# Kernel tuning notes

Measured on AMD Instinct MI355X. Metric: run time of the kernel, lower is better.

Reference implementation:

```python
import jax, jax.numpy as jnp
import numpy as np

DIM = 2048
N_HEADS = 16
N_KV_HEADS = 4
HEAD_DIM = 128
SLIDING_WINDOW = 1024
ROPE_BASE = 10000.0


def _rotate_half(x):
    d = x.shape[-1] // 2
    return jnp.concatenate((-x[..., d:], x[..., :d]), axis=-1)


def _rope_cos_sin(T, dtype):
    inv_freq = 1.0 / (ROPE_BASE ** (jnp.arange(0, HEAD_DIM, 2, dtype=jnp.float32) / HEAD_DIM))
    t = jnp.arange(T, dtype=jnp.float32)
    freqs = jnp.outer(t, inv_freq)            # [T, HEAD_DIM//2]
    emb = jnp.concatenate((freqs, freqs), axis=-1)  # [T, HEAD_DIM]
    return jnp.cos(emb).astype(dtype), jnp.sin(emb).astype(dtype)


def setup_inputs() -> dict:
    key = jax.random.key(0)
    kx, kq, kk, kv, ko = jax.random.split(key, 5)
    s_in = 1.0 / np.sqrt(DIM)
    s_o = 1.0 / np.sqrt(N_HEADS * HEAD_DIM)
    return {
        "x": jax.random.normal(kx, (1, 4096, DIM), dtype=jnp.float32),
        "Wq": jax.random.normal(kq, (DIM, N_HEADS * HEAD_DIM), dtype=jnp.float32) * s_in,
        "Wk": jax.random.normal(kk, (DIM, N_KV_HEADS * HEAD_DIM), dtype=jnp.float32) * s_in,
        "Wv": jax.random.normal(kv, (DIM, N_KV_HEADS * HEAD_DIM), dtype=jnp.float32) * s_in,
        "Wo": jax.random.normal(ko, (N_HEADS * HEAD_DIM, DIM), dtype=jnp.float32) * s_o,
    }


def reference(x, Wq, Wk, Wv, Wo):
    B, T, C = x.shape
    # projections -> [B, H, T, D]
    q = (x @ Wq).reshape(B, T, N_HEADS, HEAD_DIM).transpose(0, 2, 1, 3)
    k = (x @ Wk).reshape(B, T, N_KV_HEADS, HEAD_DIM).transpose(0, 2, 1, 3)
    v = (x @ Wv).reshape(B, T, N_KV_HEADS, HEAD_DIM).transpose(0, 2, 1, 3)

    cos, sin = _rope_cos_sin(T, x.dtype)      # [T, D], broadcast over B, H
    q = q * cos + _rotate_half(q) * sin
    k = k * cos + _rotate_half(k) * sin

    # GQA: repeat kv heads (repeat_interleave over head axis)
    kv_rep = N_HEADS // N_KV_HEADS
    k = jnp.repeat(k, kv_rep, axis=1)
    v = jnp.repeat(v, kv_rep, axis=1)

    scale = 1.0 / np.sqrt(HEAD_DIM)
    att = jnp.einsum("bhqd,bhkd->bhqk", q, k) * scale  # [B, H, T, T]

    i = jnp.arange(T)[:, None]
    j = jnp.arange(T)[None, :]
    allowed = (j <= i) & ((i - j) < SLIDING_WINDOW)     # causal + sliding window
    att = jnp.where(allowed, att, -jnp.inf)
    att = jax.nn.softmax(att, axis=-1)

    y = jnp.einsum("bhqk,bhkd->bhqd", att, v)           # [B, H, T, D]
    y = y.transpose(0, 2, 1, 3).reshape(B, T, N_HEADS * HEAD_DIM)
    return y @ Wo
```

## Files before the change

kernel.cpp:

```cpp
#include <hip/hip_runtime.h>
#include <math.h>

typedef __bf16 bf16;
typedef __bf16 bf16x8 __attribute__((ext_vector_type(8)));
typedef __bf16 bf16x4 __attribute__((ext_vector_type(4)));
typedef float f32x4 __attribute__((ext_vector_type(4)));

__device__ __forceinline__ void ldg_lds16(const bf16* g, bf16* l) {
#if __has_builtin(__builtin_amdgcn_global_load_lds)
    __builtin_amdgcn_global_load_lds(
        (const __attribute__((address_space(1))) void*)g,
        (__attribute__((address_space(3))) void*)l, 16, 0, 0);
#else
    *(bf16x8*)l = *(const bf16x8*)g;
#endif
}

__global__ void cvt_x(const float* __restrict__ X, bf16* __restrict__ Xb, int total8)
{
    int idx = blockIdx.x * 256 + threadIdx.x;
    if (idx >= total8) return;
    const float* p = X + (size_t)idx * 8;
    f32x4 a = *reinterpret_cast<const f32x4*>(p);
    f32x4 b = *reinterpret_cast<const f32x4*>(p + 4);
    bf16x8 r;
    r[0] = (bf16)a[0]; r[1] = (bf16)a[1]; r[2] = (bf16)a[2]; r[3] = (bf16)a[3];
    r[4] = (bf16)b[0]; r[5] = (bf16)b[1]; r[6] = (bf16)b[2]; r[7] = (bf16)b[3];
    *reinterpret_cast<bf16x8*>(Xb + (size_t)idx * 8) = r;
}

__global__ void cvt_wt3(const float* __restrict__ Wq, const float* __restrict__ Wk,
                        const float* __restrict__ Wv, bf16* __restrict__ Wt)
{
    __shared__ float t[32][33];
    int bx = blockIdx.x;
    const float* W; int Ncols, nbase;
    if (bx < 64)      { W = Wq; Ncols = 2048; nbase = 0;    }
    else if (bx < 80) { W = Wk; Ncols = 512;  nbase = 2048; bx -= 64; }
    else              { W = Wv; Ncols = 512;  nbase = 2560; bx -= 80; }
    const int n0 = bx * 32, k0 = blockIdx.y * 32;
    const int x = threadIdx.x, y = threadIdx.y;
    #pragma unroll
    for (int i = 0; i < 4; ++i)
        t[y + 8 * i][x] = W[(size_t)(k0 + y + 8 * i) * Ncols + n0 + x];
    __syncthreads();
    #pragma unroll
    for (int i = 0; i < 4; ++i)
        Wt[(size_t)(nbase + n0 + y + 8 * i) * 2048 + k0 + x] = (bf16)t[x][y + 8 * i];
}

__global__ void cvt_wt(const float* __restrict__ W, bf16* __restrict__ Wt, int Ncols)
{
    __shared__ float t[32][33];
    const int n0 = blockIdx.x * 32, k0 = blockIdx.y * 32;
    const int x = threadIdx.x, y = threadIdx.y;
    #pragma unroll
    for (int i = 0; i < 4; ++i)
        t[y + 8 * i][x] = W[(size_t)(k0 + y + 8 * i) * Ncols + n0 + x];
    __syncthreads();
    #pragma unroll
    for (int i = 0; i < 4; ++i)
        Wt[(size_t)(n0 + y + 8 * i) * 2048 + k0 + x] = (bf16)t[x][y + 8 * i];
}

template <int MODE>
__global__ __launch_bounds__(256) void gemm_bt(
    const bf16* __restrict__ A, const bf16* __restrict__ Bt,
    void* __restrict__ C0, void* __restrict__ C1, void* __restrict__ C2,
    int M, int N, int K)
{
    __shared__ __align__(16) bf16 As[128 * 32];
    __shared__ __align__(16) bf16 Bs[128 * 32];

    const int tid  = threadIdx.x;
    const int lane = tid & 63;
    const int wave = tid >> 6;
    const int quad = lane >> 4;
    const int l16  = lane & 15;

    const int m0 = blockIdx.y * 128;
    const int n0 = blockIdx.x * 128;
    const int wm = (wave >> 1) * 64;
    const int wn = (wave & 1) * 64;

    f32x4 acc[4][4] = {};

    for (int k0 = 0; k0 < K; k0 += 32) {
        #pragma unroll
        for (int p = 0; p < 2; ++p) {
            int u = p * 256 + tid;
            int row = u >> 2, kc = u & 3;
            ldg_lds16(A  + (size_t)(m0 + row) * K + k0 + kc * 8, &As[u * 8]);
            ldg_lds16(Bt + (size_t)(n0 + row) * K + k0 + kc * 8, &Bs[u * 8]);
        }
        __syncthreads();

        bf16x8 af[4], bfr[4];
        #pragma unroll
        for (int i = 0; i < 4; ++i) {
            af[i]  = *reinterpret_cast<const bf16x8*>(&As[(wm + i * 16 + l16) * 32 + quad * 8]);
            bfr[i] = *reinterpret_cast<const bf16x8*>(&Bs[(wn + i * 16 + l16) * 32 + quad * 8]);
        }
        #pragma unroll
        for (int mi = 0; mi < 4; ++mi)
            #pragma unroll
            for (int ni = 0; ni < 4; ++ni)
                acc[mi][ni] = __builtin_amdgcn_mfma_f32_16x16x32_bf16(
                    af[mi], bfr[ni], acc[mi][ni], 0, 0, 0);
        __syncthreads();
    }

    #pragma unroll
    for (int mi = 0; mi < 4; ++mi) {
        #pragma unroll
        for (int ni = 0; ni < 4; ++ni) {
            const int row = m0 + wm + mi * 16 + quad * 4;
            const int col = n0 + wn + ni * 16 + l16;
            if (MODE == 2) {
                float* C = (float*)C0;
                #pragma unroll
                for (int r = 0; r < 4; ++r)
                    C[(size_t)(row + r) * N + col] = acc[mi][ni][r];
            } else {
                if (n0 < 2048) {
                    bf16* Q = (bf16*)C0;
                    #pragma unroll
                    for (int r = 0; r < 4; ++r)
                        Q[(size_t)(row + r) * 2048 + col] = (bf16)acc[mi][ni][r];
                } else if (n0 < 2560) {
                    bf16* Kb = (bf16*)C1;
                    #pragma unroll
                    for (int r = 0; r < 4; ++r)
                        Kb[(size_t)(row + r) * 512 + (col - 2048)] = (bf16)acc[mi][ni][r];
                } else {
                    bf16* Vt = (bf16*)C2;
                    bf16x4 v;
                    #pragma unroll
                    for (int r = 0; r < 4; ++r) v[r] = (bf16)acc[mi][ni][r];
                    *reinterpret_cast<bf16x4*>(&Vt[(size_t)(col - 2560) * 4096 + row]) = v;
                }
            }
        }
    }
}

__global__ __launch_bounds__(512, 2) void gemm256_qkv(
    const bf16* __restrict__ A, const bf16* __restrict__ Bt,
    bf16* __restrict__ Qo, bf16* __restrict__ Ko, bf16* __restrict__ Vt,
    int K)
{
    __shared__ __align__(16) bf16 smem[2 * 32768];

    const int tid  = threadIdx.x;
    const int lane = tid & 63;
    const int wave = tid >> 6;
    const int quad = lane >> 4;
    const int l16  = lane & 15;
    const int wm   = wave >> 2;
    const int wn   = wave & 3;

    const int m0 = blockIdx.y * 256;
    const int n0 = blockIdx.x * 256;

    int offA[4], offB[4];
    #pragma unroll
    for (int p = 0; p < 4; ++p) {
        int u = p * 512 + tid;
        int row = u >> 3;
        int kc8 = (u & 7) ^ (row & 7);
        offA[p] = (m0 + row) * K + kc8 * 8;
        offB[p] = (n0 + row) * K + kc8 * 8;
    }
    const int dstoff = tid * 8;

    const int xv = (l16 & 7) << 4;
    const int c0 = ((quad * 16) ^ xv) >> 1;
    const int c1 = ((64 + quad * 16) ^ xv) >> 1;
    const int rA = (wm * 128 + l16) * 64;
    const int rB = (wn * 64 + l16) * 64;

    f32x4 acc[8][4] = {};
    const int NT = K >> 6;

    {
        bf16* d0 = smem;
        bf16* d1 = smem + 32768;
        #pragma unroll
        for (int p = 0; p < 4; ++p) {
            ldg_lds16(A  + offA[p], d0 + p * 4096 + dstoff);
            ldg_lds16(Bt + offB[p], d0 + 16384 + p * 4096 + dstoff);
        }
        #pragma unroll
        for (int p = 0; p < 4; ++p) {
            ldg_lds16(A  + offA[p] + 64, d1 + p * 4096 + dstoff);
            ldg_lds16(Bt + offB[p] + 64, d1 + 16384 + p * 4096 + dstoff);
        }
    }
    asm volatile("s_waitcnt vmcnt(8)" ::: "memory");
    __builtin_amdgcn_sched_barrier(0);
    __builtin_amdgcn_s_barrier();
    __builtin_amdgcn_sched_barrier(0);

    for (int t = 0; t < NT; ++t) {
        const bf16* As = smem + (t & 1) * 32768;
        const bf16* Bs = As + 16384;

        bf16x8 a0[8], b0[4];
        #pragma unroll
        for (int i = 0; i < 8; ++i)
            a0[i] = *(const bf16x8*)(As + rA + i * 1024 + c0);
        #pragma unroll
        for (int i = 0; i < 4; ++i)
            b0[i] = *(const bf16x8*)(Bs + rB + i * 1024 + c0);

        #pragma unroll
        for (int mi = 0; mi < 8; ++mi)
            #pragma unroll
            for (int ni = 0; ni < 4; ++ni)
                acc[mi][ni] = __builtin_amdgcn_mfma_f32_16x16x32_bf16(
                    a0[mi], b0[ni], acc[mi][ni], 0, 0, 0);

        bf16x8 a1[8], b1[4];
        #pragma unroll
        for (int i = 0; i < 8; ++i)
            a1[i] = *(const bf16x8*)(As + rA + i * 1024 + c1);
        #pragma unroll
        for (int i = 0; i < 4; ++i)
            b1[i] = *(const bf16x8*)(Bs + rB + i * 1024 + c1);

        asm volatile("s_waitcnt lgkmcnt(0)" ::: "memory");
        __builtin_amdgcn_sched_barrier(0);
        __builtin_amdgcn_s_barrier();
        __builtin_amdgcn_sched_barrier(0);

        if (t + 2 < NT) {
            bf16* d = smem + (t & 1) * 32768;
            const int koff = (t + 2) * 64;
            #pragma unroll
            for (int p = 0; p < 4; ++p) {
                ldg_lds16(A  + offA[p] + koff, d + p * 4096 + dstoff);
                ldg_lds16(Bt + offB[p] + koff, d + 16384 + p * 4096 + dstoff);
            }
        }

        __builtin_amdgcn_s_setprio(1);
        #pragma unroll
        for (int mi = 0; mi < 8; ++mi)
            #pragma unroll
            for (int ni = 0; ni < 4; ++ni)
                acc[mi][ni] = __builtin_amdgcn_mfma_f32_16x16x32_bf16(
                    a1[mi], b1[ni], acc[mi][ni], 0, 0, 0);
        __builtin_amdgcn_s_setprio(0);

        if (t + 2 < NT) {
            asm volatile("s_waitcnt vmcnt(8)" ::: "memory");
            __builtin_amdgcn_sched_barrier(0);
            __builtin_amdgcn_s_barrier();
            __builtin_amdgcn_sched_barrier(0);
        } else if (t == NT - 2) {
            asm volatile("s_waitcnt vmcnt(0)" ::: "memory");
            __builtin_amdgcn_sched_barrier(0);
            __builtin_amdgcn_s_barrier();
            __builtin_amdgcn_sched_barrier(0);
        }
    }

    #pragma unroll
    for (int mi = 0; mi < 8; ++mi) {
        #pragma unroll
        for (int ni = 0; ni < 4; ++ni) {
            const int row = m0 + wm * 128 + mi * 16 + quad * 4;
            const int col = n0 + wn * 64 + ni * 16 + l16;
            if (n0 < 2048) {
                #pragma unroll
                for (int r = 0; r < 4; ++r)
                    Qo[(size_t)(row + r) * 2048 + col] = (bf16)acc[mi][ni][r];
            } else if (n0 < 2560) {
                #pragma unroll
                for (int r = 0; r < 4; ++r)
                    Ko[(size_t)(row + r) * 512 + (col - 2048)] = (bf16)acc[mi][ni][r];
            } else {
                bf16x4 v;
                #pragma unroll
                for (int r = 0; r < 4; ++r) v[r] = (bf16)acc[mi][ni][r];
                *reinterpret_cast<bf16x4*>(&Vt[(size_t)(col - 2560) * 4096 + row]) = v;
            }
        }
    }
}

__global__ void rope2_kernel(bf16* __restrict__ Qb, bf16* __restrict__ Kb,
                             int qtot, int ktot)
{
    int idx = blockIdx.x * 256 + threadIdx.x;
    bf16* base; int logH;
    if (idx < qtot) { base = Qb; logH = 4; }
    else {
        idx -= qtot;
        if (idx >= ktot) return;
        base = Kb; logH = 2;
    }
    int j  = idx & 63;
    int th = idx >> 6;
    int t  = th >> logH;

    bf16* p = base + (size_t)th * 128;
    const float NEG_LN1E4_64 = -0.14391155806323211f;
    float inv_freq = expf(NEG_LN1E4_64 * (float)j);
    float ang = (float)t * inv_freq;
    float c = cosf(ang), s = sinf(ang);
    float q0 = (float)p[j], q1 = (float)p[j + 64];
    p[j]      = (bf16)(q0 * c - q1 * s);
    p[j + 64] = (bf16)(q1 * c + q0 * s);
}

__global__ __launch_bounds__(256) void attn_v7(
    const bf16* __restrict__ Q, const bf16* __restrict__ K,
    const bf16* __restrict__ Vt, bf16* __restrict__ Y)
{
    const float scale = 0.08838834764831845f;

    __shared__ __align__(16) bf16 Ks[2 * 64 * 128];
    __shared__ __align__(16) bf16 Vs[2 * 128 * 64];
    __shared__ __align__(16) bf16 Pl[4][16 * 72];

    const int tid  = threadIdx.x;
    const int lane = tid & 63;
    const int wave = tid >> 6;
    const int quad = lane >> 4;
    const int l16  = lane & 15;

    const int i0  = blockIdx.x * 64;
    const int h   = blockIdx.y;
    const int kvh = h >> 2;
    const int q0  = i0 + wave * 16;
    bf16* Plw = Pl[wave];

    bf16x8 qf[4];
    {
        const bf16* qp = Q + (size_t)(q0 + l16) * 2048 + h * 128 + quad * 8;
        #pragma unroll
        for (int c = 0; c < 4; ++c)
            qf[c] = *reinterpret_cast<const bf16x8*>(qp + c * 32);
    }

    f32x4 o[8] = {};
    float lsum[4] = {0.f, 0.f, 0.f, 0.f};

    const int ks = (i0 >= 1024) ? (i0 - 1024) : 0;
    const int nsteps = (i0 + 64 - ks) >> 6;

    auto stage = [&](int tt, int bsel) {
        const int k0s = ks + tt * 64;
        bf16* kd = Ks + bsel * 8192;
        bf16* vd = Vs + bsel * 8192;
        #pragma unroll
        for (int p = 0; p < 4; ++p) {
            int u = p * 256 + tid;
            int kk = u >> 4, sc = u & 15;
            ldg_lds16(K + (size_t)(k0s + kk) * 512 + kvh * 128 + (sc ^ (kk & 15)) * 8,
                      kd + u * 8);
        }
        #pragma unroll
        for (int p = 0; p < 4; ++p) {
            int u = p * 256 + tid;
            int d = u >> 3, sc = u & 7;
            ldg_lds16(Vt + (size_t)(kvh * 128 + d) * 4096 + k0s + (sc ^ (d & 7)) * 8,
                      vd + u * 8);
        }
    };

    stage(0, 0);
    stage(1, 1);
    asm volatile("s_waitcnt vmcnt(8)" ::: "memory");
    __builtin_amdgcn_sched_barrier(0);
    __builtin_amdgcn_s_barrier();
    __builtin_amdgcn_sched_barrier(0);

    for (int t = 0; t < nsteps; ++t) {
        const int b  = t & 1;
        const int k0 = ks + t * 64;
        const bf16* Kb = Ks + b * 8192;
        const bf16* Vb = Vs + b * 8192;

        f32x4 s[4];
        __builtin_amdgcn_s_setprio(1);
        #pragma unroll
        for (int kh = 0; kh < 4; ++kh) {
            const int kk = kh * 16 + l16;
            f32x4 sv = {};
            #pragma unroll
            for (int c = 0; c < 4; ++c) {
                bf16x8 kf = *reinterpret_cast<const bf16x8*>(
                    &Kb[kk * 128 + (((c * 4 + quad) ^ (kk & 15)) * 8)]);
                sv = __builtin_amdgcn_mfma_f32_16x16x32_bf16(qf[c], kf, sv, 0, 0, 0);
            }
            s[kh] = sv;
        }
        __builtin_amdgcn_s_setprio(0);

        #pragma unroll
        for (int kh = 0; kh < 4; ++kh) {
            const int key = k0 + kh * 16 + l16;
            #pragma unroll
            for (int r = 0; r < 4; ++r) {
                const int qrow = q0 + quad * 4 + r;
                bool ok = (unsigned)(qrow - key) < 1024u;
                float pv = ok ? __expf(s[kh][r] * scale) : 0.f;
                lsum[r] += pv;
                Plw[(quad * 4 + r) * 72 + kh * 16 + l16] = (bf16)pv;
            }
        }

        bf16x8 pf0 = *reinterpret_cast<const bf16x8*>(&Plw[l16 * 72 + quad * 8]);
        bf16x8 pf1 = *reinterpret_cast<const bf16x8*>(&Plw[l16 * 72 + 32 + quad * 8]);
        __builtin_amdgcn_s_setprio(1);
        #pragma unroll
        for (int n = 0; n < 8; ++n) {
            const int d = n * 16 + l16;
            bf16x8 v0 = *reinterpret_cast<const bf16x8*>(
                &Vb[d * 64 + (((quad) ^ (d & 7)) * 8)]);
            bf16x8 v1 = *reinterpret_cast<const bf16x8*>(
                &Vb[d * 64 + (((4 + quad) ^ (d & 7)) * 8)]);
            o[n] = __builtin_amdgcn_mfma_f32_16x16x32_bf16(pf0, v0, o[n], 0, 0, 0);
            o[n] = __builtin_amdgcn_mfma_f32_16x16x32_bf16(pf1, v1, o[n], 0, 0, 0);
        }
        __builtin_amdgcn_s_setprio(0);

        asm volatile("s_waitcnt lgkmcnt(0)" ::: "memory");
        __builtin_amdgcn_sched_barrier(0);
        __builtin_amdgcn_s_barrier();
        __builtin_amdgcn_sched_barrier(0);

        if (t + 2 < nsteps) {
            stage(t + 2, b);
            asm volatile("s_waitcnt vmcnt(8)" ::: "memory");
        } else {
            asm volatile("s_waitcnt vmcnt(0)" ::: "memory");
        }
        __builtin_amdgcn_sched_barrier(0);
        __builtin_amdgcn_s_barrier();
        __builtin_amdgcn_sched_barrier(0);
    }

    #pragma unroll
    for (int r = 0; r < 4; ++r) {
        #pragma unroll
        for (int off = 1; off < 16; off <<= 1)
            lsum[r] += __shfl_xor(lsum[r], off, 64);
    }
    #pragma unroll
    for (int r = 0; r < 4; ++r) {
        int row = q0 + quad * 4 + r;
        float inv = (lsum[r] > 0.f) ? 1.f / lsum[r] : 0.f;
        #pragma unroll
        for (int n = 0; n < 8; ++n)
            Y[(size_t)row * 2048 + h * 128 + n * 16 + l16] = (bf16)(o[n][r] * inv);
    }
}

extern "C" void kernel_launch(void* const* d_in, const int* in_sizes, int n_in,
                              void* d_out, int out_size, void* d_ws, size_t ws_size,
                              hipStream_t stream)
{
    const float* x  = (const float*)d_in[0];
    const float* Wq = (const float*)d_in[1];
    const float* Wk = (const float*)d_in[2];
    const float* Wv = (const float*)d_in[3];
    const float* Wo = (const float*)d_in[4];
    float* out = (float*)d_out;

    const int T = 4096, DIM = 2048;

    char* po = (char*)d_out;
    bf16* Qb = (bf16*)(po);
    bf16* Kb = (bf16*)(po + (16u << 20));
    bf16* Vtb = (bf16*)(po + (20u << 20));

    char* ws = (char*)d_ws;
    bf16* xb    = (bf16*)(ws);
    bf16* Wqkvt = (bf16*)(ws + (16u << 20));
    bf16* Yb    = (bf16*)(ws);
    bf16* Wot   = (bf16*)(ws + (16u << 20));

    cvt_x<<<dim3(T * DIM / 8 / 256), 256, 0, stream>>>(x, xb, T * DIM / 8);

    dim3 tb(32, 8);
    cvt_wt3<<<dim3(96, 64), tb, 0, stream>>>(Wq, Wk, Wv, Wqkvt);

    gemm256_qkv<<<dim3(3072 / 256, T / 256), 512, 0, stream>>>(
        xb, Wqkvt, Qb, Kb, Vtb, DIM);

    cvt_wt<<<dim3(2048 / 32, 64), tb, 0, stream>>>(Wo, Wot, 2048);

    int qtot = T * 16 * 64, ktot = T * 4 * 64;
    rope2_kernel<<<(qtot + ktot + 255) / 256, 256, 0, stream>>>(Qb, Kb, qtot, ktot);

    attn_v7<<<dim3(T / 64, 16), 256, 0, stream>>>(Qb, Kb, Vtb, Yb);

    gemm_bt<2><<<dim3(2048 / 128, T / 128), 256, 0, stream>>>(
        Yb, Wot, out, nullptr, nullptr, T, 2048, DIM);
}
```

Baseline: 317.3 us.

## Replace output projection GEMM with double-buffered swizzled 256x128 kernel; reverse attention block order

The output projection moves from a simple single-buffered 128x128 GEMM to a 512-thread 256x128 tile kernel. The new kernel uses a 64-wide K step, an XOR-swizzled LDS layout, double buffering with direct global-to-LDS loads, and explicit waitcnt/barrier scheduling with setprio around the MFMA blocks. The aim is to hide global load latency and cut LDS bank conflicts. The attention kernel also launches query tiles in reverse order, so the longer sliding-window blocks are scheduled first and tail imbalance shrinks. The larger tile halves the grid to 256 blocks and raises register and LDS pressure.

```diff
diff --git a/kernel.cpp b/kernel.cpp
--- a/kernel.cpp
+++ b/kernel.cpp
@@ -61,87 +61,6 @@
     #pragma unroll
     for (int i = 0; i < 4; ++i)
         Wt[(size_t)(n0 + y + 8 * i) * 2048 + k0 + x] = (bf16)t[x][y + 8 * i];
-}
-
-template <int MODE>
-__global__ __launch_bounds__(256) void gemm_bt(
-    const bf16* __restrict__ A, const bf16* __restrict__ Bt,
-    void* __restrict__ C0, void* __restrict__ C1, void* __restrict__ C2,
-    int M, int N, int K)
-{
-    __shared__ __align__(16) bf16 As[128 * 32];
-    __shared__ __align__(16) bf16 Bs[128 * 32];
-
-    const int tid  = threadIdx.x;
-    const int lane = tid & 63;
-    const int wave = tid >> 6;
-    const int quad = lane >> 4;
-    const int l16  = lane & 15;
-
-    const int m0 = blockIdx.y * 128;
-    const int n0 = blockIdx.x * 128;
-    const int wm = (wave >> 1) * 64;
-    const int wn = (wave & 1) * 64;
-
-    f32x4 acc[4][4] = {};
-
-    for (int k0 = 0; k0 < K; k0 += 32) {
-        #pragma unroll
-        for (int p = 0; p < 2; ++p) {
-            int u = p * 256 + tid;
-            int row = u >> 2, kc = u & 3;
-            ldg_lds16(A  + (size_t)(m0 + row) * K + k0 + kc * 8, &As[u * 8]);
-            ldg_lds16(Bt + (size_t)(n0 + row) * K + k0 + kc * 8, &Bs[u * 8]);
-        }
-        __syncthreads();
-
-        bf16x8 af[4], bfr[4];
-        #pragma unroll
-        for (int i = 0; i < 4; ++i) {
-            af[i]  = *reinterpret_cast<const bf16x8*>(&As[(wm + i * 16 + l16) * 32 + quad * 8]);
-            bfr[i] = *reinterpret_cast<const bf16x8*>(&Bs[(wn + i * 16 + l16) * 32 + quad * 8]);
-        }
-        #pragma unroll
-        for (int mi = 0; mi < 4; ++mi)
-            #pragma unroll
-            for (int ni = 0; ni < 4; ++ni)
-                acc[mi][ni] = __builtin_amdgcn_mfma_f32_16x16x32_bf16(
-                    af[mi], bfr[ni], acc[mi][ni], 0, 0, 0);
-        __syncthreads();
-    }
-
-    #pragma unroll
-    for (int mi = 0; mi < 4; ++mi) {
-        #pragma unroll
-        for (int ni = 0; ni < 4; ++ni) {
-            const int row = m0 + wm + mi * 16 + quad * 4;
-            const int col = n0 + wn + ni * 16 + l16;
-            if (MODE == 2) {
-                float* C = (float*)C0;
-                #pragma unroll
-                for (int r = 0; r < 4; ++r)
-                    C[(size_t)(row + r) * N + col] = acc[mi][ni][r];
-            } else {
-                if (n0 < 2048) {
-                    bf16* Q = (bf16*)C0;
-                    #pragma unroll
-                    for (int r = 0; r < 4; ++r)
-                        Q[(size_t)(row + r) * 2048 + col] = (bf16)acc[mi][ni][r];
-                } else if (n0 < 2560) {
-                    bf16* Kb = (bf16*)C1;
-                    #pragma unroll
-                    for (int r = 0; r < 4; ++r)
-                        Kb[(size_t)(row + r) * 512 + (col - 2048)] = (bf16)acc[mi][ni][r];
-                } else {
-                    bf16* Vt = (bf16*)C2;
-                    bf16x4 v;
-                    #pragma unroll
-                    for (int r = 0; r < 4; ++r) v[r] = (bf16)acc[mi][ni][r];
-                    *reinterpret_cast<bf16x4*>(&Vt[(size_t)(col - 2560) * 4096 + row]) = v;
-                }
-            }
-        }
-    }
 }
 
 __global__ __launch_bounds__(512, 2) void gemm256_qkv(
@@ -289,6 +208,137 @@
     }
 }
 
+__global__ __launch_bounds__(512, 2) void gemm_out(
+    const bf16* __restrict__ A, const bf16* __restrict__ Bt,
+    float* __restrict__ C, int K)
+{
+    __shared__ __align__(16) bf16 smem[2 * 24576];
+
+    const int tid  = threadIdx.x;
+    const int lane = tid & 63;
+    const int wave = tid >> 6;
+    const int quad = lane >> 4;
+    const int l16  = lane & 15;
+    const int wm   = wave >> 1;
+    const int wn   = wave & 1;
+
+    const int m0 = blockIdx.y * 256;
+    const int n0 = blockIdx.x * 128;
+
+    int offA[4], offB[2];
+    #pragma unroll
+    for (int p = 0; p < 4; ++p) {
+        int u = p * 512 + tid;
+        int row = u >> 3;
+        int kc8 = (u & 7) ^ (row & 7);
+        offA[p] = (m0 + row) * K + kc8 * 8;
+    }
+    #pragma unroll
+    for (int p = 0; p < 2; ++p) {
+        int u = p * 512 + tid;
+        int row = u >> 3;
+        int kc8 = (u & 7) ^ (row & 7);
+        offB[p] = (n0 + row) * K + kc8 * 8;
+    }
+    const int dstoff = tid * 8;
+
+    const int xv = (l16 & 7) << 4;
+    const int c0 = ((quad * 16) ^ xv) >> 1;
+    const int c1 = ((64 + quad * 16) ^ xv) >> 1;
+    const int rA = (wm * 64 + l16) * 64;
+    const int rB = (wn * 64 + l16) * 64;
+
+    f32x4 acc[4][4] = {};
+    const int NT = K >> 6;
+
+    auto stage = [&](int tt, int bsel) {
+        bf16* as = smem + bsel * 24576;
+        bf16* bs = as + 16384;
+        const int koff = tt * 64;
+        #pragma unroll
+        for (int p = 0; p < 4; ++p)
+            ldg_lds16(A + offA[p] + koff, as + p * 4096 + dstoff);
+        #pragma unroll
+        for (int p = 0; p < 2; ++p)
+            ldg_lds16(Bt + offB[p] + koff, bs + p * 4096 + dstoff);
+    };
+
+    stage(0, 0);
+    stage(1, 1);
+    asm volatile("s_waitcnt vmcnt(6)" ::: "memory");
+    __builtin_amdgcn_sched_barrier(0);
+    __builtin_amdgcn_s_barrier();
+    __builtin_amdgcn_sched_barrier(0);
+
+    for (int t = 0; t < NT; ++t) {
+        const bf16* As = smem + (t & 1) * 24576;
+        const bf16* Bs = As + 16384;
+
+        bf16x8 a0[4], b0[4];
+        #pragma unroll
+        for (int i = 0; i < 4; ++i)
+            a0[i] = *(const bf16x8*)(As + rA + i * 1024 + c0);
+        #pragma unroll
+        for (int i = 0; i < 4; ++i)
+            b0[i] = *(const bf16x8*)(Bs + rB + i * 1024 + c0);
+
+        #pragma unroll
+        for (int mi = 0; mi < 4; ++mi)
+            #pragma unroll
+            for (int ni = 0; ni < 4; ++ni)
+                acc[mi][ni] = __builtin_amdgcn_mfma_f32_16x16x32_bf16(
+                    a0[mi], b0[ni], acc[mi][ni], 0, 0, 0);
+
+        bf16x8 a1[4], b1[4];
+        #pragma unroll
+        for (int i = 0; i < 4; ++i)
+            a1[i] = *(const bf16x8*)(As + rA + i * 1024 + c1);
+        #pragma unroll
+        for (int i = 0; i < 4; ++i)
+            b1[i] = *(const bf16x8*)(Bs + rB + i * 1024 + c1);
+
+        asm volatile("s_waitcnt lgkmcnt(0)" ::: "memory");
+        __builtin_amdgcn_sched_barrier(0);
+        __builtin_amdgcn_s_barrier();
+        __builtin_amdgcn_sched_barrier(0);
+
+        if (t + 2 < NT) stage(t + 2, t & 1);
+
+        __builtin_amdgcn_s_setprio(1);
+        #pragma unroll
+        for (int mi = 0; mi < 4; ++mi)
+            #pragma unroll
+            for (int ni = 0; ni < 4; ++ni)
+                acc[mi][ni] = __builtin_amdgcn_mfma_f32_16x16x32_bf16(
+                    a1[mi], b1[ni], acc[mi][ni], 0, 0, 0);
+        __builtin_amdgcn_s_setprio(0);
+
+        if (t + 2 < NT) {
+            asm volatile("s_waitcnt vmcnt(6)" ::: "memory");
+            __builtin_amdgcn_sched_barrier(0);
+            __builtin_amdgcn_s_barrier();
+            __builtin_amdgcn_sched_barrier(0);
+        } else if (t == NT - 2) {
+            asm volatile("s_waitcnt vmcnt(0)" ::: "memory");
+            __builtin_amdgcn_sched_barrier(0);
+            __builtin_amdgcn_s_barrier();
+            __builtin_amdgcn_sched_barrier(0);
+        }
+    }
+
+    #pragma unroll
+    for (int mi = 0; mi < 4; ++mi) {
+        #pragma unroll
+        for (int ni = 0; ni < 4; ++ni) {
+            const int row = m0 + wm * 64 + mi * 16 + quad * 4;
+            const int col = n0 + wn * 64 + ni * 16 + l16;
+            #pragma unroll
+            for (int r = 0; r < 4; ++r)
+                C[(size_t)(row + r) * 2048 + col] = acc[mi][ni][r];
+        }
+    }
+}
+
 __global__ void rope2_kernel(bf16* __restrict__ Qb, bf16* __restrict__ Kb,
                              int qtot, int ktot)
 {
@@ -330,7 +380,7 @@
     const int quad = lane >> 4;
     const int l16  = lane & 15;
 
-    const int i0  = blockIdx.x * 64;
+    const int i0  = (gridDim.x - 1 - blockIdx.x) * 64;
     const int h   = blockIdx.y;
     const int kvh = h >> 2;
     const int q0  = i0 + wave * 16;
@@ -498,6 +548,6 @@
 
     attn_v7<<<dim3(T / 64, 16), 256, 0, stream>>>(Qb, Kb, Vtb, Yb);
 
-    gemm_bt<2><<<dim3(2048 / 128, T / 128), 256, 0, stream>>>(
-        Yb, Wot, out, nullptr, nullptr, T, 2048, DIM);
-}
+    gemm_out<<<dim3(2048 / 128, T / 256), 512, 0, stream>>>(
+        Yb, Wot, out, DIM);
+}
```

Result: faster. 297.2 us (-6.3%).
